# Performance work log

Measured on AMD Instinct MI355X. Metric: run time of the kernel, lower is better.

Reference implementation:

```python
import jax, jax.numpy as jnp
from jax import lax
import numpy as np

DN = ('NCHW', 'OIHW', 'NCHW')


def conv(x, w, b, pad=0):
    y = lax.conv_general_dilated(x, w, (1, 1), [(pad, pad), (pad, pad)],
                                 dimension_numbers=DN)
    return y + b[None, :, None, None]


def deconv(x, w, b, stride=1):
    # PyTorch ConvTranspose2d weight is (in, out, kH, kW); equivalent conv uses
    # flipped, in/out-transposed kernel with lhs dilation = stride, pad = k-1.
    k = w.shape[2]
    wt = jnp.flip(w, (2, 3)).transpose(1, 0, 2, 3)
    y = lax.conv_general_dilated(x, wt, (1, 1), [(k - 1, k - 1), (k - 1, k - 1)],
                                 lhs_dilation=(stride, stride), dimension_numbers=DN)
    return y + b[None, :, None, None]


def maxpool2(x):
    return lax.reduce_window(x, -jnp.inf, lax.max, (1, 1, 2, 2), (1, 1, 2, 2), 'VALID')


def setup_inputs() -> dict:
    key = jax.random.key(0)
    ks = jax.random.split(key, 12)
    B = 256

    def he(k, shape, fan_in):
        return jax.random.normal(k, shape, jnp.float32) * np.sqrt(2.0 / fan_in)

    inp = {
        'x': jax.random.normal(ks[0], (B, 1, 28, 28), jnp.float32),
        # encoder convs
        'w1': he(ks[1], (128, 1, 5, 5), 1 * 25), 'b1': jnp.zeros((128,), jnp.float32),
        'w2': he(ks[2], (128, 128, 5, 5), 128 * 25), 'b2': jnp.zeros((128,), jnp.float32),
        'w3': he(ks[3], (128, 128, 5, 5), 128 * 25), 'b3': jnp.zeros((128,), jnp.float32),
        # decoder transposed convs (torch shape: in, out, kH, kW)
        't1w': he(ks[4], (128, 128, 4, 4), 128 * 16), 't1b': jnp.zeros((128,), jnp.float32),
        't2w': he(ks[5], (128, 128, 4, 4), 128 * 16), 't2b': jnp.zeros((128,), jnp.float32),
        't3w': he(ks[6], (128, 128, 5, 5), 128 * 25), 't3b': jnp.zeros((128,), jnp.float32),
        't4w': he(ks[7], (128, 128, 5, 5), 128 * 25), 't4b': jnp.zeros((128,), jnp.float32),
        # mu_net 1x1 conv
        'mw': he(ks[8], (1, 128, 1, 1), 128), 'mb': jnp.zeros((1,), jnp.float32),
        # codebook: Embedding(128, 128), init ~ N(0, 1)
        'dict_w': jax.random.normal(ks[9], (128, 128), jnp.float32),
    }
    return inp


def reference(x, w1, b1, w2, b2, w3, b3,
              t1w, t1b, t2w, t2b, t3w, t3b, t4w, t4b,
              mw, mb, dict_w):
    BETA, RATE = 0.25, 5.0
    # ---- encoder ----
    h = jax.nn.relu(conv(x, w1, b1, pad=0))          # (B,128,24,24)
    h = jax.nn.relu(conv(h, w2, b2, pad=2))          # (B,128,24,24)
    h = maxpool2(h)                                  # (B,128,12,12)
    h = conv(h, w3, b3, pad=2)                       # (B,128,12,12)
    z = maxpool2(h)                                  # (B,128,6,6)

    # ---- nearest_neighbor (faithful: argmax of distance, as in the source) ----
    z_sg = lax.stop_gradient(z)
    z2 = jnp.sum(z_sg * z_sg, axis=1, keepdims=True)          # (B,1,6,6)
    w2n = jnp.sum(dict_w * dict_w, axis=1)                     # (K,)
    cross = jnp.einsum('bchw,kc->bkhw', z_sg, lax.stop_gradient(dict_w))
    d2 = z2 + w2n[None, :, None, None] - 2.0 * cross           # (B,K,6,6)
    index = jnp.argmax(d2, axis=1)                             # (B,6,6) int

    # ---- embedding gather ----
    val = dict_w[index].transpose(0, 3, 1, 2)                  # (B,128,6,6)

    # ---- decoder on detached codes ----
    f = lax.stop_gradient(val)
    f = jax.nn.relu(deconv(f, t1w, t1b, stride=1))             # (B,128,9,9)
    f = jax.nn.relu(deconv(f, t2w, t2b, stride=2))             # (B,128,20,20)
    f = jax.nn.relu(deconv(f, t3w, t3b, stride=1))             # (B,128,24,24)
    f = jax.nn.relu(deconv(f, t4w, t4b, stride=1))             # (B,128,28,28)
    mu = conv(f, mw, mb, pad=0)                                # (B,1,28,28)

    loss_rec = jnp.mean((mu - x) ** 2)
    dict_loss = jnp.mean((val - lax.stop_gradient(z)) ** 2) * RATE
    enc_loss = jnp.mean((z - lax.stop_gradient(val)) ** 2) * BETA * RATE
    var_loss = jnp.zeros((), jnp.float32)
    losses = jnp.stack([loss_rec, dict_loss, enc_loss, var_loss])
    return losses, index
```

## Files before the change

kernel.cpp:

```cpp
#include <hip/hip_runtime.h>
#include <hip/hip_bf16.h>


#define B_ 256

typedef __attribute__((ext_vector_type(8))) short s16x8;
typedef __attribute__((ext_vector_type(4))) short s16x4;
typedef __attribute__((ext_vector_type(8))) _Float16 f16x8;
typedef __attribute__((ext_vector_type(4))) float f32x4;

__device__ inline ushort f2bf(float f) {
  union { __hip_bfloat16 h; ushort u; } cv;
  cv.h = __float2bfloat16(f);
  return cv.u;
}

__global__ __launch_bounds__(256) void prep_w(const float* __restrict__ w,
                                              ushort* __restrict__ wp,
                                              int K2) {
  int idx = blockIdx.x * 256 + threadIdx.x;
  if (idx >= K2 * 16384) return;
  int ci = idx & 127;
  int co = (idx >> 7) & 127;
  int tap = idx >> 14;
  wp[idx] = f2bf(w[((size_t)ci * 128 + co) * K2 + (K2 - 1 - tap)]);
}

__global__ __launch_bounds__(256) void prep_w_s2(const float* __restrict__ w,
                                                 ushort* __restrict__ wp) {
  int idx = blockIdx.x * 256 + threadIdx.x;
  int ci = idx & 127;
  int co = (idx >> 7) & 127;
  int tap = (idx >> 14) & 3;
  int pp = idx >> 16;
  int u = tap >> 1, v = tap & 1;
  int py = pp >> 1, px = pp & 1;
  wp[idx] =
      f2bf(w[(((size_t)ci * 128 + co) * 4 + (py + 2 * u)) * 4 + (px + 2 * v)]);
}

__global__ __launch_bounds__(256) void prep_w_split(const float* __restrict__ w,
                                                    _Float16* __restrict__ wh,
                                                    _Float16* __restrict__ wl,
                                                    int K2) {
  int idx = blockIdx.x * 256 + threadIdx.x;
  if (idx >= K2 * 16384) return;
  int ci = idx & 127;
  int co = (idx >> 7) & 127;
  int tap = idx >> 14;
  float v = w[((size_t)co * 128 + ci) * K2 + tap];
  _Float16 h = (_Float16)v;
  wh[idx] = h;
  wl[idx] = (_Float16)(v - (float)h);
}

__global__ __launch_bounds__(256) void conv1_kernel(
    const float* __restrict__ x, const float* __restrict__ w,
    const float* __restrict__ b, _Float16* __restrict__ oh,
    _Float16* __restrict__ ol) {
  const int n = blockIdx.x;
  __shared__ float xl[784];
  __shared__ float wl[128 * 25];
  __shared__ float bl[128];
  const int t = threadIdx.x;
  for (int e = t; e < 784; e += 256) xl[e] = x[n * 784 + e];
  for (int e = t; e < 3200; e += 256) wl[e] = w[e];
  if (t < 128) bl[t] = b[t];
  __syncthreads();
  const size_t nb = (size_t)n * 73728;
  for (int idx = t; idx < 73728; idx += 256) {
    int co = idx & 127, p = idx >> 7;
    int y = p / 24, xx = p % 24;
    float acc = bl[co];
    const float* wc = &wl[co * 25];
#pragma unroll
    for (int ky = 0; ky < 5; ky++)
#pragma unroll
      for (int kx = 0; kx < 5; kx++)
        acc += xl[(y + ky) * 28 + xx + kx] * wc[ky * 5 + kx];
    float v = fmaxf(acc, 0.f);
    _Float16 h = (_Float16)v;
    oh[nb + idx] = h;
    ol[nb + idx] = (_Float16)(v - (float)h);
  }
}

template <int IW, int K, int PAD, int TR, bool RELU, bool OUT_F32>
__global__ __launch_bounds__(256, 3) void conv_mfma_pool(
    const _Float16* __restrict__ inh, const _Float16* __restrict__ inl,
    const _Float16* __restrict__ wph, const _Float16* __restrict__ wpl,
    const float* __restrict__ bias, _Float16* __restrict__ outh,
    _Float16* __restrict__ outl, float* __restrict__ outf) {
  constexpr int IH = IW, OW = IW, OH = IW;
  constexpr int PW = IW + 2 * PAD;
  constexpr int SROWS = TR + K - 1;
  constexpr int S = SROWS * PW;
  constexpr int NPOS = TR * OW;
  constexpr int NCH = NPOS / 16;
  constexpr int K2 = K * K;
  constexpr int PITCH = 40;
  constexpr int LIN_ELT = S * PITCH;
  constexpr int LIN_BYTES = 2 * LIN_ELT * 2;
  constexpr int SCR_BYTES = 64 * NPOS * 4;
  constexpr int SMEM_BYTES = LIN_BYTES > SCR_BYTES ? LIN_BYTES : SCR_BYTES;
  static_assert(NPOS % 16 == 0, "");
  static_assert(TR % 2 == 0 && OW % 2 == 0, "");
  __shared__ __align__(16) char smem[SMEM_BYTES];
  _Float16* linh = (_Float16*)smem;
  _Float16* linl = linh + LIN_ELT;
  const int n = blockIdx.x;
  const int r0 = blockIdx.y * TR;
  const int t = threadIdx.x;
  const int wv = t >> 6;
  const int lane = t & 63;
  const int nn = lane & 15;
  const int q = lane >> 4;
  f32x4 acc0[NCH], acc1[NCH];
#pragma unroll
  for (int c = 0; c < NCH; c++) {
    acc0[c] = f32x4{0.f, 0.f, 0.f, 0.f};
    acc1[c] = f32x4{0.f, 0.f, 0.f, 0.f};
  }
  int base[NCH];
#pragma unroll
  for (int c = 0; c < NCH; c++) {
    int p = c * 16 + nn;
    base[c] = (p / OW) * PW + (p % OW);
  }
  const int rowA = wv * 16 + nn;
  const int rowB = (wv + 4) * 16 + nn;
  for (int cb = 0; cb < 4; cb++) {
    const int ci0 = cb * 32;
    __syncthreads();
    for (int e = t; e < S * 4; e += 256) {
      int sp = e >> 2, j = e & 3;
      int r = sp / PW, c = sp - r * PW;
      int ir = r0 + r - PAD, ic = c - PAD;
      f16x8 vh = {0, 0, 0, 0, 0, 0, 0, 0};
      f16x8 vl = {0, 0, 0, 0, 0, 0, 0, 0};
      if (ir >= 0 && ir < IH && ic >= 0 && ic < IW) {
        size_t g = ((size_t)n * (IH * IW) + ir * IW + ic) * 128 + ci0 + j * 8;
        vh = *(const f16x8*)&inh[g];
        vl = *(const f16x8*)&inl[g];
      }
      int st = sp * PITCH + ((j + (sp >> 3)) & 3) * 8;
      *(f16x8*)&linh[st] = vh;
      *(f16x8*)&linl[st] = vl;
    }
    __syncthreads();
    const size_t gA = (size_t)rowA * 128 + ci0 + q * 8;
    const size_t gB = (size_t)rowB * 128 + ci0 + q * 8;
    f16x8 cah0 = *(const f16x8*)&wph[gA];
    f16x8 cal0 = *(const f16x8*)&wpl[gA];
    f16x8 cah1 = *(const f16x8*)&wph[gB];
    f16x8 cal1 = *(const f16x8*)&wpl[gB];
    for (int tap = 0; tap < K2; tap++) {
      f16x8 nah0 = cah0, nal0 = cal0, nah1 = cah1, nal1 = cal1;
      if (tap + 1 < K2) {
        size_t oA = gA + (size_t)(tap + 1) * 16384;
        size_t oB = gB + (size_t)(tap + 1) * 16384;
        nah0 = *(const f16x8*)&wph[oA];
        nal0 = *(const f16x8*)&wpl[oA];
        nah1 = *(const f16x8*)&wph[oB];
        nal1 = *(const f16x8*)&wpl[oB];
      }
      const int ky = tap / K, kx = tap - ky * K;
      const int toff = ky * PW + kx;
#pragma unroll
      for (int c = 0; c < NCH; c++) {
        int s = base[c] + toff;
        int off = s * PITCH + ((q + (s >> 3)) & 3) * 8;
        f16x8 bh = *(const f16x8*)&linh[off];
        f16x8 bl = *(const f16x8*)&linl[off];
        acc0[c] =
            __builtin_amdgcn_mfma_f32_16x16x32_f16(cah0, bh, acc0[c], 0, 0, 0);
        acc0[c] =
            __builtin_amdgcn_mfma_f32_16x16x32_f16(cah0, bl, acc0[c], 0, 0, 0);
        acc0[c] =
            __builtin_amdgcn_mfma_f32_16x16x32_f16(cal0, bh, acc0[c], 0, 0, 0);
        acc1[c] =
            __builtin_amdgcn_mfma_f32_16x16x32_f16(cah1, bh, acc1[c], 0, 0, 0);
        acc1[c] =
            __builtin_amdgcn_mfma_f32_16x16x32_f16(cah1, bl, acc1[c], 0, 0, 0);
        acc1[c] =
            __builtin_amdgcn_mfma_f32_16x16x32_f16(cal1, bh, acc1[c], 0, 0, 0);
      }
      cah0 = nah0; cal0 = nal0; cah1 = nah1; cal1 = nal1;
    }
  }
  __syncthreads();
  float* scr = (float*)smem + wv * 16 * NPOS;
#pragma unroll
  for (int j = 0; j < 2; j++) {
    const int cot = (j ? wv + 4 : wv) * 16;
#pragma unroll
    for (int c = 0; c < NCH; c++) {
      f32x4 a = j ? acc1[c] : acc0[c];
#pragma unroll
      for (int r = 0; r < 4; r++) {
        float v = a[r] + bias[cot + q * 4 + r];
        if (RELU) v = fmaxf(v, 0.f);
        scr[(q * 4 + r) * NPOS + c * 16 + nn] = v;
      }
    }
    __syncthreads();
    for (int e = lane; e < 16 * (TR / 2) * (OW / 2); e += 64) {
      int co_l = e & 15;
      int rem = e >> 4;
      int pr = rem / (OW / 2), pc = rem - pr * (OW / 2);
      const float* s = scr + co_l * NPOS;
      int lp = (2 * pr) * OW + 2 * pc;
      float m =
          fmaxf(fmaxf(s[lp], s[lp + 1]), fmaxf(s[lp + OW], s[lp + OW + 1]));
      int sp_out = (r0 / 2 + pr) * (OW / 2) + pc;
      size_t go = ((size_t)n * ((OH / 2) * (OW / 2)) + sp_out) * 128 + cot + co_l;
      if (OUT_F32) {
        outf[go] = m;
      } else {
        _Float16 h = (_Float16)m;
        outh[go] = h;
        outl[go] = (_Float16)(m - (float)h);
      }
    }
    __syncthreads();
  }
}

__global__ __launch_bounds__(256) void vq_kernel(
    const float* __restrict__ z, const float* __restrict__ dict,
    float* __restrict__ val, ushort* __restrict__ val_bf,
    float* __restrict__ out_idx) {
  const int n = blockIdx.x;
  __shared__ float zl[36 * 128];
  __shared__ float d2[36 * 129];
  __shared__ float w2n[128];
  __shared__ int bk[36];
  const int t = threadIdx.x;
  const float* zn = z + (size_t)n * 4608;
  for (int e = t; e < 4608; e += 256) zl[e] = zn[e];
  if (t < 128) {
    float s = 0.f;
    const float* wr = dict + t * 128;
    for (int c = 0; c < 128; c++) s += wr[c] * wr[c];
    w2n[t] = s;
  }
  __syncthreads();
  const int k = t & 127, pg = t >> 7;
  float dot[18];
#pragma unroll
  for (int i = 0; i < 18; i++) dot[i] = 0.f;
  const float* wr = dict + k * 128;
  for (int c = 0; c < 128; c++) {
    float wv = wr[c];
#pragma unroll
    for (int i = 0; i < 18; i++) dot[i] += zl[(pg * 18 + i) * 128 + c] * wv;
  }
  float wn = w2n[k];
#pragma unroll
  for (int i = 0; i < 18; i++) d2[(pg * 18 + i) * 129 + k] = wn - 2.f * dot[i];
  __syncthreads();
  if (t < 36) {
    const float* dr = &d2[t * 129];
    float best = dr[0];
    int bi = 0;
    for (int kk = 1; kk < 128; kk++) {
      float v = dr[kk];
      if (v > best) { best = v; bi = kk; }
    }
    bk[t] = bi;
    out_idx[n * 36 + t] = (float)bi;
  }
  __syncthreads();
  float* vn = val + (size_t)n * 4608;
  ushort* vbn = val_bf + (size_t)n * 4608;
  for (int e = t; e < 4608; e += 256) {
    int c = e & 127, p = e >> 7;
    float v = dict[bk[p] * 128 + c];
    vn[e] = v;
    vbn[e] = f2bf(v);
  }
}

template <int IH, int IW, int OH, int OW, int K, int TR, bool MU_FUSE>
__global__ __launch_bounds__(256, 3) void deconv_mfma(
    const ushort* __restrict__ in, const ushort* __restrict__ wprep,
    const float* __restrict__ bias, const float* __restrict__ mw,
    void* __restrict__ outp) {
  constexpr int PAD = K - 1;
  constexpr int PW = IW + 2 * PAD;
  constexpr int K2 = K * K;
  constexpr int SROWS = TR + K - 1;
  constexpr int S = SROWS * PW;
  constexpr int NPOS = TR * OW;
  constexpr int NCH = (NPOS + 15) / 16;
  constexpr int PITCH = 40;
  const int n = blockIdx.x;
  const int r0 = blockIdx.y * TR;
  __shared__ __align__(16) ushort lin[S * PITCH];
  const int t = threadIdx.x;
  const int wv = t >> 6;
  const int lane = t & 63;
  const int nn = lane & 15;
  const int q = lane >> 4;
  f32x4 acc0[NCH], acc1[NCH];
  int base[NCH];
#pragma unroll
  for (int c = 0; c < NCH; c++) {
    acc0[c] = f32x4{0.f, 0.f, 0.f, 0.f};
    acc1[c] = f32x4{0.f, 0.f, 0.f, 0.f};
    int p = c * 16 + nn;
    int pc = p < NPOS ? p : NPOS - 1;
    base[c] = (pc / OW) * PW + (pc % OW);
  }
  for (int cb = 0; cb < 4; cb++) {
    const int ci0 = cb * 32;
    __syncthreads();
    for (int e = t; e < S * 4; e += 256) {
      int sp = e >> 2, j = e & 3;
      int rr = sp / PW, cc = sp - rr * PW;
      int ir = r0 + rr - PAD, ic = cc - PAD;
      s16x8 v = {0, 0, 0, 0, 0, 0, 0, 0};
      if (ir >= 0 && ir < IH && ic >= 0 && ic < IW)
        v = *(const s16x8*)&in[((size_t)n * (IH * IW) + ir * IW + ic) * 128 +
                               ci0 + j * 8];
      *(s16x8*)&lin[sp * PITCH + ((j + (sp >> 3)) & 3) * 8] = v;
    }
    __syncthreads();
    const size_t gA = (size_t)(wv * 16 + nn) * 128 + ci0 + q * 8;
    const size_t gB = (size_t)((wv + 4) * 16 + nn) * 128 + ci0 + q * 8;
    s16x8 ca0 = *(const s16x8*)&wprep[gA];
    s16x8 ca1 = *(const s16x8*)&wprep[gB];
    for (int tap = 0; tap < K2; tap++) {
      s16x8 na0 = ca0, na1 = ca1;
      if (tap + 1 < K2) {
        na0 = *(const s16x8*)&wprep[gA + (size_t)(tap + 1) * 16384];
        na1 = *(const s16x8*)&wprep[gB + (size_t)(tap + 1) * 16384];
      }
      const int ky = tap / K, kx = tap - ky * K;
      const int toff = ky * PW + kx;
#pragma unroll
      for (int c = 0; c < NCH; c++) {
        int s = base[c] + toff;
        s16x8 b = *(const s16x8*)&lin[s * PITCH + ((q + (s >> 3)) & 3) * 8];
        acc0[c] =
            __builtin_amdgcn_mfma_f32_16x16x32_bf16(ca0, b, acc0[c], 0, 0, 0);
        acc1[c] =
            __builtin_amdgcn_mfma_f32_16x16x32_bf16(ca1, b, acc1[c], 0, 0, 0);
      }
      ca0 = na0; ca1 = na1;
    }
  }
  const int co_a = wv * 16 + q * 4;
  const int co_b = (wv + 4) * 16 + q * 4;
  float ba[4], bb[4];
#pragma unroll
  for (int r = 0; r < 4; r++) {
    ba[r] = bias[co_a + r];
    bb[r] = bias[co_b + r];
  }
  if (!MU_FUSE) {
    ushort* out = (ushort*)outp;
#pragma unroll
    for (int c = 0; c < NCH; c++) {
      int p = c * 16 + nn;
      if (p < NPOS) {
        size_t go = ((size_t)n * (OH * OW) + r0 * OW + p) * 128;
        s16x4 pa, pb;
#pragma unroll
        for (int r = 0; r < 4; r++) {
          pa[r] = (short)f2bf(fmaxf(acc0[c][r] + ba[r], 0.f));
          pb[r] = (short)f2bf(fmaxf(acc1[c][r] + bb[r], 0.f));
        }
        *(s16x4*)&out[go + co_a] = pa;
        *(s16x4*)&out[go + co_b] = pb;
      }
    }
  } else {
    float* out = (float*)outp;
    float wa[4], wb[4];
#pragma unroll
    for (int r = 0; r < 4; r++) {
      wa[r] = mw[co_a + r];
      wb[r] = mw[co_b + r];
    }
#pragma unroll
    for (int c = 0; c < NCH; c++) {
      int p = c * 16 + nn;
      float s = 0.f;
#pragma unroll
      for (int r = 0; r < 4; r++) {
        s += fmaxf(acc0[c][r] + ba[r], 0.f) * wa[r];
        s += fmaxf(acc1[c][r] + bb[r], 0.f) * wb[r];
      }
      s += __shfl_xor(s, 16);
      s += __shfl_xor(s, 32);
      if (q == 0 && p < NPOS)
        atomicAdd(&out[(size_t)n * (OH * OW) + r0 * OW + p], s);
    }
  }
}

__global__ __launch_bounds__(256, 3) void deconv_s2_mfma(
    const ushort* __restrict__ in, const ushort* __restrict__ wp2,
    const float* __restrict__ bias, ushort* __restrict__ out) {
  constexpr int NCH = 7;
  constexpr int PITCH = 40;
  const int n = blockIdx.x;
  const int pp = blockIdx.y;
  const int py = pp >> 1, px = pp & 1;
  __shared__ __align__(16) ushort lin[121 * PITCH];
  const int t = threadIdx.x;
  const int wv = t >> 6;
  const int lane = t & 63;
  const int nn = lane & 15;
  const int q = lane >> 4;
  f32x4 acc0[NCH], acc1[NCH];
  int base[NCH];
#pragma unroll
  for (int c = 0; c < NCH; c++) {
    acc0[c] = f32x4{0.f, 0.f, 0.f, 0.f};
    acc1[c] = f32x4{0.f, 0.f, 0.f, 0.f};
    int p = c * 16 + nn;
    int pc = p < 100 ? p : 99;
    base[c] = (pc / 10) * 11 + (pc % 10);
  }
  const int toffs[4] = {12, 11, 1, 0};
  for (int cb = 0; cb < 4; cb++) {
    const int ci0 = cb * 32;
    __syncthreads();
    for (int e = t; e < 121 * 4; e += 256) {
      int sp = e >> 2, j = e & 3;
      int r = sp / 11, c2 = sp - r * 11;
      int ir = r - 1, ic = c2 - 1;
      s16x8 v = {0, 0, 0, 0, 0, 0, 0, 0};
      if (ir >= 0 && ir < 9 && ic >= 0 && ic < 9)
        v = *(const s16x8*)&in[((size_t)n * 81 + ir * 9 + ic) * 128 + ci0 +
                               j * 8];
      *(s16x8*)&lin[sp * PITCH + ((j + (sp >> 3)) & 3) * 8] = v;
    }
    __syncthreads();
    const size_t gA =
        ((size_t)(pp * 4) * 128 + wv * 16 + nn) * 128 + ci0 + q * 8;
    const size_t gB =
        ((size_t)(pp * 4) * 128 + (wv + 4) * 16 + nn) * 128 + ci0 + q * 8;
    s16x8 ca0 = *(const s16x8*)&wp2[gA];
    s16x8 ca1 = *(const s16x8*)&wp2[gB];
    for (int tap = 0; tap < 4; tap++) {
      s16x8 na0 = ca0, na1 = ca1;
      if (tap + 1 < 4) {
        na0 = *(const s16x8*)&wp2[gA + (size_t)(tap + 1) * 16384];
        na1 = *(const s16x8*)&wp2[gB + (size_t)(tap + 1) * 16384];
      }
      const int toff = toffs[tap];
#pragma unroll
      for (int c = 0; c < NCH; c++) {
        int s = base[c] + toff;
        s16x8 b = *(const s16x8*)&lin[s * PITCH + ((q + (s >> 3)) & 3) * 8];
        acc0[c] =
            __builtin_amdgcn_mfma_f32_16x16x32_bf16(ca0, b, acc0[c], 0, 0, 0);
        acc1[c] =
            __builtin_amdgcn_mfma_f32_16x16x32_bf16(ca1, b, acc1[c], 0, 0, 0);
      }
      ca0 = na0; ca1 = na1;
    }
  }
  const int co_a = wv * 16 + q * 4;
  const int co_b = (wv + 4) * 16 + q * 4;
#pragma unroll
  for (int c = 0; c < NCH; c++) {
    int p = c * 16 + nn;
    if (p < 100) {
      int oy = 2 * (p / 10) + py, ox = 2 * (p % 10) + px;
      size_t go = ((size_t)n * 400 + oy * 20 + ox) * 128;
      s16x4 pa, pb;
#pragma unroll
      for (int r = 0; r < 4; r++) {
        pa[r] = (short)f2bf(fmaxf(acc0[c][r] + bias[co_a + r], 0.f));
        pb[r] = (short)f2bf(fmaxf(acc1[c][r] + bias[co_b + r], 0.f));
      }
      *(s16x4*)&out[go + co_a] = pa;
      *(s16x4*)&out[go + co_b] = pb;
    }
  }
}

__global__ __launch_bounds__(256) void rec_loss_kernel(
    const float* __restrict__ mu, const float* __restrict__ mb,
    const float* __restrict__ x, float* __restrict__ out) {
  const int t = threadIdx.x;
  const int i = blockIdx.x * 256 + t;
  __shared__ float red[256];
  float d = mu[i] + mb[0] - x[i];
  red[t] = d * d;
  __syncthreads();
  for (int off = 128; off > 0; off >>= 1) {
    if (t < off) red[t] += red[t + off];
    __syncthreads();
  }
  if (t == 0) atomicAdd(out, red[0] * (1.0f / 200704.f));
}

__global__ __launch_bounds__(256) void vq_loss_kernel(
    const float4* __restrict__ val4, const float4* __restrict__ z4,
    float* __restrict__ out) {
  const int t = threadIdx.x;
  const int i = blockIdx.x * 256 + t;
  __shared__ float red[256];
  float4 a = val4[i], b = z4[i];
  float dx = a.x - b.x, dy = a.y - b.y, dz = a.z - b.z, dw = a.w - b.w;
  red[t] = dx * dx + dy * dy + dz * dz + dw * dw;
  __syncthreads();
  for (int off = 128; off > 0; off >>= 1) {
    if (t < off) red[t] += red[t + off];
    __syncthreads();
  }
  if (t == 0) {
    atomicAdd(out + 1, red[0] * (5.f / 1179648.f));
    atomicAdd(out + 2, red[0] * (1.25f / 1179648.f));
  }
}

extern "C" void kernel_launch(void* const* d_in, const int* in_sizes, int n_in,
                              void* d_out, int out_size, void* d_ws,
                              size_t ws_size, hipStream_t stream) {
  const float* x = (const float*)d_in[0];
  const float* w1 = (const float*)d_in[1];
  const float* b1 = (const float*)d_in[2];
  const float* w2 = (const float*)d_in[3];
  const float* b2 = (const float*)d_in[4];
  const float* w3 = (const float*)d_in[5];
  const float* b3 = (const float*)d_in[6];
  const float* t1w = (const float*)d_in[7];
  const float* t1b = (const float*)d_in[8];
  const float* t2w = (const float*)d_in[9];
  const float* t2b = (const float*)d_in[10];
  const float* t3w = (const float*)d_in[11];
  const float* t3b = (const float*)d_in[12];
  const float* t4w = (const float*)d_in[13];
  const float* t4b = (const float*)d_in[14];
  const float* mw = (const float*)d_in[15];
  const float* mb = (const float*)d_in[16];
  const float* dictw = (const float*)d_in[17];
  float* out = (float*)d_out;

  float* p = (float*)d_ws;
  _Float16* h1h = (_Float16*)p; p += 9437184;
  _Float16* h1l = (_Float16*)p; p += 9437184;
  _Float16* p1h = (_Float16*)p; p += 2359296;
  _Float16* p1l = (_Float16*)p; p += 2359296;
  float* z = p; p += 1179648;
  float* val = p; p += 1179648;
  ushort* val_bf = (ushort*)p; p += 589824;
  float* mu = p; p += 200704;
  ushort* wp1 = (ushort*)p; p += 131072;
  ushort* wp3 = (ushort*)p; p += 204800;
  ushort* wp4 = (ushort*)p; p += 204800;
  ushort* wp2 = (ushort*)p; p += 131072;
  _Float16* w2h = (_Float16*)p; p += 204800;
  _Float16* w2l = (_Float16*)p; p += 204800;
  _Float16* w3h = (_Float16*)p; p += 204800;
  _Float16* w3l = (_Float16*)p; p += 204800;
  ushort* f1 = (ushort*)p1h;
  ushort* f2 = (ushort*)h1l;
  ushort* f3 = (ushort*)h1h;

  hipMemsetAsync(d_out, 0, 4 * sizeof(float), stream);
  hipMemsetAsync(mu, 0, 200704 * sizeof(float), stream);

  prep_w<<<16 * 64, 256, 0, stream>>>(t1w, wp1, 16);
  prep_w<<<25 * 64, 256, 0, stream>>>(t3w, wp3, 25);
  prep_w<<<25 * 64, 256, 0, stream>>>(t4w, wp4, 25);
  prep_w_s2<<<1024, 256, 0, stream>>>(t2w, wp2);
  prep_w_split<<<25 * 64, 256, 0, stream>>>(w2, w2h, w2l, 25);
  prep_w_split<<<25 * 64, 256, 0, stream>>>(w3, w3h, w3l, 25);

  conv1_kernel<<<B_, 256, 0, stream>>>(x, w1, b1, h1h, h1l);
  conv_mfma_pool<24, 5, 2, 6, true, false>
      <<<dim3(B_, 4), 256, 0, stream>>>(h1h, h1l, w2h, w2l, b2, p1h, p1l,
                                        nullptr);
  conv_mfma_pool<12, 5, 2, 4, false, true>
      <<<dim3(B_, 3), 256, 0, stream>>>(p1h, p1l, w3h, w3l, b3, nullptr,
                                        nullptr, z);
  vq_kernel<<<B_, 256, 0, stream>>>(z, dictw, val, val_bf, out + 4);
  deconv_mfma<6, 6, 9, 9, 4, 9, false>
      <<<dim3(B_, 1), 256, 0, stream>>>(val_bf, wp1, t1b, nullptr, f1);
  deconv_s2_mfma<<<dim3(B_, 4), 256, 0, stream>>>(f1, wp2, t2b, f2);
  deconv_mfma<20, 20, 24, 24, 5, 8, false>
      <<<dim3(B_, 3), 256, 0, stream>>>(f2, wp3, t3b, nullptr, f3);
  deconv_mfma<24, 24, 28, 28, 5, 7, true>
      <<<dim3(B_, 4), 256, 0, stream>>>(f3, wp4, t4b, mw, mu);
  rec_loss_kernel<<<784, 256, 0, stream>>>(mu, mb, x, out);
  vq_loss_kernel<<<1152, 256, 0, stream>>>((const float4*)val, (const float4*)z,
                                           out);
}
```

Baseline: 1.011 ms.

## Double-buffer LDS input staging in conv/deconv, merge prep and loss kernels

The conv and deconv MFMA kernels now prefetch the next 32-channel input slice into registers while computing on the current slice, then store it into a second LDS buffer. This removes one barrier per channel block and overlaps global loads with MFMA work. Launch bounds drop from 3 to 2 blocks per SM to make room for the doubled shared memory and staging registers. Conv2 switches from 6-row to 4-row tiles, and the six weight-prep kernels and the two loss kernels are each merged into one launch. Together these cut launch overhead at some cost in occupancy.

```diff
diff --git a/kernel.cpp b/kernel.cpp
--- a/kernel.cpp
+++ b/kernel.cpp
@@ -15,43 +15,49 @@
   return cv.u;
 }
 
-__global__ __launch_bounds__(256) void prep_w(const float* __restrict__ w,
-                                              ushort* __restrict__ wp,
-                                              int K2) {
-  int idx = blockIdx.x * 256 + threadIdx.x;
-  if (idx >= K2 * 16384) return;
-  int ci = idx & 127;
-  int co = (idx >> 7) & 127;
-  int tap = idx >> 14;
-  wp[idx] = f2bf(w[((size_t)ci * 128 + co) * K2 + (K2 - 1 - tap)]);
-}
-
-__global__ __launch_bounds__(256) void prep_w_s2(const float* __restrict__ w,
-                                                 ushort* __restrict__ wp) {
-  int idx = blockIdx.x * 256 + threadIdx.x;
-  int ci = idx & 127;
-  int co = (idx >> 7) & 127;
-  int tap = (idx >> 14) & 3;
-  int pp = idx >> 16;
-  int u = tap >> 1, v = tap & 1;
-  int py = pp >> 1, px = pp & 1;
-  wp[idx] =
-      f2bf(w[(((size_t)ci * 128 + co) * 4 + (py + 2 * u)) * 4 + (px + 2 * v)]);
-}
-
-__global__ __launch_bounds__(256) void prep_w_split(const float* __restrict__ w,
-                                                    _Float16* __restrict__ wh,
-                                                    _Float16* __restrict__ wl,
-                                                    int K2) {
-  int idx = blockIdx.x * 256 + threadIdx.x;
-  if (idx >= K2 * 16384) return;
-  int ci = idx & 127;
-  int co = (idx >> 7) & 127;
-  int tap = idx >> 14;
-  float v = w[((size_t)co * 128 + ci) * K2 + tap];
-  _Float16 h = (_Float16)v;
-  wh[idx] = h;
-  wl[idx] = (_Float16)(v - (float)h);
+__global__ __launch_bounds__(256) void prep_all(
+    const float* __restrict__ t1w, const float* __restrict__ t3w,
+    const float* __restrict__ t4w, const float* __restrict__ t2w,
+    const float* __restrict__ w2, const float* __restrict__ w3,
+    ushort* __restrict__ wp1, ushort* __restrict__ wp3,
+    ushort* __restrict__ wp4, ushort* __restrict__ wp2,
+    _Float16* __restrict__ w2h, _Float16* __restrict__ w2l,
+    _Float16* __restrict__ w3h, _Float16* __restrict__ w3l) {
+  const int b = blockIdx.x, t = threadIdx.x;
+  if (b < 1024) {
+    int idx = b * 256 + t;
+    int ci = idx & 127, co = (idx >> 7) & 127, tap = idx >> 14;
+    wp1[idx] = f2bf(t1w[((size_t)ci * 128 + co) * 16 + (15 - tap)]);
+  } else if (b < 2624) {
+    int idx = (b - 1024) * 256 + t;
+    int ci = idx & 127, co = (idx >> 7) & 127, tap = idx >> 14;
+    wp3[idx] = f2bf(t3w[((size_t)ci * 128 + co) * 25 + (24 - tap)]);
+  } else if (b < 4224) {
+    int idx = (b - 2624) * 256 + t;
+    int ci = idx & 127, co = (idx >> 7) & 127, tap = idx >> 14;
+    wp4[idx] = f2bf(t4w[((size_t)ci * 128 + co) * 25 + (24 - tap)]);
+  } else if (b < 5248) {
+    int idx = (b - 4224) * 256 + t;
+    int ci = idx & 127, co = (idx >> 7) & 127;
+    int tap = (idx >> 14) & 3, pp = idx >> 16;
+    int u = tap >> 1, v = tap & 1, py = pp >> 1, px = pp & 1;
+    wp2[idx] = f2bf(
+        t2w[(((size_t)ci * 128 + co) * 4 + (py + 2 * u)) * 4 + (px + 2 * v)]);
+  } else if (b < 6848) {
+    int idx = (b - 5248) * 256 + t;
+    int ci = idx & 127, co = (idx >> 7) & 127, tap = idx >> 14;
+    float v = w2[((size_t)co * 128 + ci) * 25 + tap];
+    _Float16 h = (_Float16)v;
+    w2h[idx] = h;
+    w2l[idx] = (_Float16)(v - (float)h);
+  } else {
+    int idx = (b - 6848) * 256 + t;
+    int ci = idx & 127, co = (idx >> 7) & 127, tap = idx >> 14;
+    float v = w3[((size_t)co * 128 + ci) * 25 + tap];
+    _Float16 h = (_Float16)v;
+    w3h[idx] = h;
+    w3l[idx] = (_Float16)(v - (float)h);
+  }
 }
 
 __global__ __launch_bounds__(256) void conv1_kernel(
@@ -86,7 +92,7 @@
 }
 
 template <int IW, int K, int PAD, int TR, bool RELU, bool OUT_F32>
-__global__ __launch_bounds__(256, 3) void conv_mfma_pool(
+__global__ __launch_bounds__(256, 2) void conv_mfma_pool(
     const _Float16* __restrict__ inh, const _Float16* __restrict__ inl,
     const _Float16* __restrict__ wph, const _Float16* __restrict__ wpl,
     const float* __restrict__ bias, _Float16* __restrict__ outh,
@@ -100,14 +106,14 @@
   constexpr int K2 = K * K;
   constexpr int PITCH = 40;
   constexpr int LIN_ELT = S * PITCH;
-  constexpr int LIN_BYTES = 2 * LIN_ELT * 2;
+  constexpr int BUF_BYTES = 2 * LIN_ELT * 2;
+  constexpr int LIN_BYTES = 2 * BUF_BYTES;
   constexpr int SCR_BYTES = 64 * NPOS * 4;
   constexpr int SMEM_BYTES = LIN_BYTES > SCR_BYTES ? LIN_BYTES : SCR_BYTES;
+  constexpr int NSTG = (S * 4 + 255) / 256;
   static_assert(NPOS % 16 == 0, "");
   static_assert(TR % 2 == 0 && OW % 2 == 0, "");
   __shared__ __align__(16) char smem[SMEM_BYTES];
-  _Float16* linh = (_Float16*)smem;
-  _Float16* linl = linh + LIN_ELT;
   const int n = blockIdx.x;
   const int r0 = blockIdx.y * TR;
   const int t = threadIdx.x;
@@ -129,25 +135,51 @@
   }
   const int rowA = wv * 16 + nn;
   const int rowB = (wv + 4) * 16 + nn;
+  f16x8 sh[NSTG], sl[NSTG];
+
+  auto load_stage = [&](int ci0) {
+#pragma unroll
+    for (int i = 0; i < NSTG; i++) {
+      int e = t + i * 256;
+      f16x8 vh = {0, 0, 0, 0, 0, 0, 0, 0};
+      f16x8 vl = {0, 0, 0, 0, 0, 0, 0, 0};
+      if (e < S * 4) {
+        int sp = e >> 2, j = e & 3;
+        int r = sp / PW, c = sp - r * PW;
+        int ir = r0 + r - PAD, ic = c - PAD;
+        if (ir >= 0 && ir < IH && ic >= 0 && ic < IW) {
+          size_t g = ((size_t)n * (IH * IW) + ir * IW + ic) * 128 + ci0 + j * 8;
+          vh = *(const f16x8*)&inh[g];
+          vl = *(const f16x8*)&inl[g];
+        }
+      }
+      sh[i] = vh;
+      sl[i] = vl;
+    }
+  };
+  auto store_stage = [&](int bsel) {
+    _Float16* lh = (_Float16*)(smem + bsel * BUF_BYTES);
+    _Float16* ll = lh + LIN_ELT;
+#pragma unroll
+    for (int i = 0; i < NSTG; i++) {
+      int e = t + i * 256;
+      if (e < S * 4) {
+        int sp = e >> 2, j = e & 3;
+        int st = sp * PITCH + ((j + (sp >> 3)) & 3) * 8;
+        *(f16x8*)&lh[st] = sh[i];
+        *(f16x8*)&ll[st] = sl[i];
+      }
+    }
+  };
+
+  load_stage(0);
+  store_stage(0);
+  __syncthreads();
   for (int cb = 0; cb < 4; cb++) {
     const int ci0 = cb * 32;
-    __syncthreads();
-    for (int e = t; e < S * 4; e += 256) {
-      int sp = e >> 2, j = e & 3;
-      int r = sp / PW, c = sp - r * PW;
-      int ir = r0 + r - PAD, ic = c - PAD;
-      f16x8 vh = {0, 0, 0, 0, 0, 0, 0, 0};
-      f16x8 vl = {0, 0, 0, 0, 0, 0, 0, 0};
-      if (ir >= 0 && ir < IH && ic >= 0 && ic < IW) {
-        size_t g = ((size_t)n * (IH * IW) + ir * IW + ic) * 128 + ci0 + j * 8;
-        vh = *(const f16x8*)&inh[g];
-        vl = *(const f16x8*)&inl[g];
-      }
-      int st = sp * PITCH + ((j + (sp >> 3)) & 3) * 8;
-      *(f16x8*)&linh[st] = vh;
-      *(f16x8*)&linl[st] = vl;
-    }
-    __syncthreads();
+    if (cb < 3) load_stage(ci0 + 32);
+    const _Float16* lh = (const _Float16*)(smem + (cb & 1) * BUF_BYTES);
+    const _Float16* ll = lh + LIN_ELT;
     const size_t gA = (size_t)rowA * 128 + ci0 + q * 8;
     const size_t gB = (size_t)rowB * 128 + ci0 + q * 8;
     f16x8 cah0 = *(const f16x8*)&wph[gA];
@@ -170,8 +202,8 @@
       for (int c = 0; c < NCH; c++) {
         int s = base[c] + toff;
         int off = s * PITCH + ((q + (s >> 3)) & 3) * 8;
-        f16x8 bh = *(const f16x8*)&linh[off];
-        f16x8 bl = *(const f16x8*)&linl[off];
+        f16x8 bh = *(const f16x8*)&lh[off];
+        f16x8 bl = *(const f16x8*)&ll[off];
         acc0[c] =
             __builtin_amdgcn_mfma_f32_16x16x32_f16(cah0, bh, acc0[c], 0, 0, 0);
         acc0[c] =
@@ -187,6 +219,10 @@
       }
       cah0 = nah0; cal0 = nal0; cah1 = nah1; cal1 = nal1;
     }
+    if (cb < 3) {
+      store_stage((cb + 1) & 1);
+      __syncthreads();
+    }
   }
   __syncthreads();
   float* scr = (float*)smem + wv * 16 * NPOS;
@@ -213,7 +249,8 @@
       float m =
           fmaxf(fmaxf(s[lp], s[lp + 1]), fmaxf(s[lp + OW], s[lp + OW + 1]));
       int sp_out = (r0 / 2 + pr) * (OW / 2) + pc;
-      size_t go = ((size_t)n * ((OH / 2) * (OW / 2)) + sp_out) * 128 + cot + co_l;
+      size_t go =
+          ((size_t)n * ((OH / 2) * (OW / 2)) + sp_out) * 128 + cot + co_l;
       if (OUT_F32) {
         outf[go] = m;
       } else {
@@ -282,7 +319,7 @@
 }
 
 template <int IH, int IW, int OH, int OW, int K, int TR, bool MU_FUSE>
-__global__ __launch_bounds__(256, 3) void deconv_mfma(
+__global__ __launch_bounds__(256, 2) void deconv_mfma(
     const ushort* __restrict__ in, const ushort* __restrict__ wprep,
     const float* __restrict__ bias, const float* __restrict__ mw,
     void* __restrict__ outp) {
@@ -294,9 +331,11 @@
   constexpr int NPOS = TR * OW;
   constexpr int NCH = (NPOS + 15) / 16;
   constexpr int PITCH = 40;
+  constexpr int LIN_ELT = S * PITCH;
+  constexpr int NSTG = (S * 4 + 255) / 256;
+  __shared__ __align__(16) ushort lin[2][LIN_ELT];
   const int n = blockIdx.x;
   const int r0 = blockIdx.y * TR;
-  __shared__ __align__(16) ushort lin[S * PITCH];
   const int t = threadIdx.x;
   const int wv = t >> 6;
   const int lane = t & 63;
@@ -312,20 +351,41 @@
     int pc = p < NPOS ? p : NPOS - 1;
     base[c] = (pc / OW) * PW + (pc % OW);
   }
+  s16x8 stg[NSTG];
+  auto load_stage = [&](int ci0) {
+#pragma unroll
+    for (int i = 0; i < NSTG; i++) {
+      int e = t + i * 256;
+      s16x8 v = {0, 0, 0, 0, 0, 0, 0, 0};
+      if (e < S * 4) {
+        int sp = e >> 2, j = e & 3;
+        int rr = sp / PW, cc = sp - rr * PW;
+        int ir = r0 + rr - PAD, ic = cc - PAD;
+        if (ir >= 0 && ir < IH && ic >= 0 && ic < IW)
+          v = *(const s16x8*)&in[((size_t)n * (IH * IW) + ir * IW + ic) * 128 +
+                                 ci0 + j * 8];
+      }
+      stg[i] = v;
+    }
+  };
+  auto store_stage = [&](int bsel) {
+#pragma unroll
+    for (int i = 0; i < NSTG; i++) {
+      int e = t + i * 256;
+      if (e < S * 4) {
+        int sp = e >> 2, j = e & 3;
+        *(s16x8*)&lin[bsel][sp * PITCH + ((j + (sp >> 3)) & 3) * 8] = stg[i];
+      }
+    }
+  };
+
+  load_stage(0);
+  store_stage(0);
+  __syncthreads();
   for (int cb = 0; cb < 4; cb++) {
     const int ci0 = cb * 32;
-    __syncthreads();
-    for (int e = t; e < S * 4; e += 256) {
-      int sp = e >> 2, j = e & 3;
-      int rr = sp / PW, cc = sp - rr * PW;
-      int ir = r0 + rr - PAD, ic = cc - PAD;
-      s16x8 v = {0, 0, 0, 0, 0, 0, 0, 0};
-      if (ir >= 0 && ir < IH && ic >= 0 && ic < IW)
-        v = *(const s16x8*)&in[((size_t)n * (IH * IW) + ir * IW + ic) * 128 +
-                               ci0 + j * 8];
-      *(s16x8*)&lin[sp * PITCH + ((j + (sp >> 3)) & 3) * 8] = v;
-    }
-    __syncthreads();
+    if (cb < 3) load_stage(ci0 + 32);
+    const ushort* L = lin[cb & 1];
     const size_t gA = (size_t)(wv * 16 + nn) * 128 + ci0 + q * 8;
     const size_t gB = (size_t)((wv + 4) * 16 + nn) * 128 + ci0 + q * 8;
     s16x8 ca0 = *(const s16x8*)&wprep[gA];
@@ -341,13 +401,17 @@
 #pragma unroll
       for (int c = 0; c < NCH; c++) {
         int s = base[c] + toff;
-        s16x8 b = *(const s16x8*)&lin[s * PITCH + ((q + (s >> 3)) & 3) * 8];
+        s16x8 b = *(const s16x8*)&L[s * PITCH + ((q + (s >> 3)) & 3) * 8];
         acc0[c] =
             __builtin_amdgcn_mfma_f32_16x16x32_bf16(ca0, b, acc0[c], 0, 0, 0);
         acc1[c] =
             __builtin_amdgcn_mfma_f32_16x16x32_bf16(ca1, b, acc1[c], 0, 0, 0);
       }
       ca0 = na0; ca1 = na1;
+    }
+    if (cb < 3) {
+      store_stage((cb + 1) & 1);
+      __syncthreads();
     }
   }
   const int co_a = wv * 16 + q * 4;
@@ -484,39 +548,34 @@
   }
 }
 
-__global__ __launch_bounds__(256) void rec_loss_kernel(
+__global__ __launch_bounds__(256) void loss_kernel(
     const float* __restrict__ mu, const float* __restrict__ mb,
-    const float* __restrict__ x, float* __restrict__ out) {
-  const int t = threadIdx.x;
-  const int i = blockIdx.x * 256 + t;
+    const float* __restrict__ x, const float4* __restrict__ val4,
+    const float4* __restrict__ z4, float* __restrict__ out) {
+  const int b = blockIdx.x, t = threadIdx.x;
   __shared__ float red[256];
-  float d = mu[i] + mb[0] - x[i];
-  red[t] = d * d;
+  if (b < 784) {
+    int i = b * 256 + t;
+    float d = mu[i] + mb[0] - x[i];
+    red[t] = d * d;
+  } else {
+    int i = (b - 784) * 256 + t;
+    float4 a = val4[i], zz = z4[i];
+    float dx = a.x - zz.x, dy = a.y - zz.y, dz = a.z - zz.z, dw = a.w - zz.w;
+    red[t] = dx * dx + dy * dy + dz * dz + dw * dw;
+  }
   __syncthreads();
   for (int off = 128; off > 0; off >>= 1) {
     if (t < off) red[t] += red[t + off];
     __syncthreads();
   }
-  if (t == 0) atomicAdd(out, red[0] * (1.0f / 200704.f));
-}
-
-__global__ __launch_bounds__(256) void vq_loss_kernel(
-    const float4* __restrict__ val4, const float4* __restrict__ z4,
-    float* __restrict__ out) {
-  const int t = threadIdx.x;
-  const int i = blockIdx.x * 256 + t;
-  __shared__ float red[256];
-  float4 a = val4[i], b = z4[i];
-  float dx = a.x - b.x, dy = a.y - b.y, dz = a.z - b.z, dw = a.w - b.w;
-  red[t] = dx * dx + dy * dy + dz * dz + dw * dw;
-  __syncthreads();
-  for (int off = 128; off > 0; off >>= 1) {
-    if (t < off) red[t] += red[t + off];
-    __syncthreads();
-  }
   if (t == 0) {
-    atomicAdd(out + 1, red[0] * (5.f / 1179648.f));
-    atomicAdd(out + 2, red[0] * (1.25f / 1179648.f));
+    if (b < 784) {
+      atomicAdd(out, red[0] * (1.0f / 200704.f));
+    } else {
+      atomicAdd(out + 1, red[0] * (5.f / 1179648.f));
+      atomicAdd(out + 2, red[0] * (1.25f / 1179648.f));
+    }
   }
 }
 
@@ -567,16 +626,12 @@
   hipMemsetAsync(d_out, 0, 4 * sizeof(float), stream);
   hipMemsetAsync(mu, 0, 200704 * sizeof(float), stream);
 
-  prep_w<<<16 * 64, 256, 0, stream>>>(t1w, wp1, 16);
-  prep_w<<<25 * 64, 256, 0, stream>>>(t3w, wp3, 25);
-  prep_w<<<25 * 64, 256, 0, stream>>>(t4w, wp4, 25);
-  prep_w_s2<<<1024, 256, 0, stream>>>(t2w, wp2);
-  prep_w_split<<<25 * 64, 256, 0, stream>>>(w2, w2h, w2l, 25);
-  prep_w_split<<<25 * 64, 256, 0, stream>>>(w3, w3h, w3l, 25);
+  prep_all<<<8448, 256, 0, stream>>>(t1w, t3w, t4w, t2w, w2, w3, wp1, wp3, wp4,
+                                     wp2, w2h, w2l, w3h, w3l);
 
   conv1_kernel<<<B_, 256, 0, stream>>>(x, w1, b1, h1h, h1l);
-  conv_mfma_pool<24, 5, 2, 6, true, false>
-      <<<dim3(B_, 4), 256, 0, stream>>>(h1h, h1l, w2h, w2l, b2, p1h, p1l,
+  conv_mfma_pool<24, 5, 2, 4, true, false>
+      <<<dim3(B_, 6), 256, 0, stream>>>(h1h, h1l, w2h, w2l, b2, p1h, p1l,
                                         nullptr);
   conv_mfma_pool<12, 5, 2, 4, false, true>
       <<<dim3(B_, 3), 256, 0, stream>>>(p1h, p1l, w3h, w3l, b3, nullptr,
@@ -589,7 +644,6 @@
       <<<dim3(B_, 3), 256, 0, stream>>>(f2, wp3, t3b, nullptr, f3);
   deconv_mfma<24, 24, 28, 28, 5, 7, true>
       <<<dim3(B_, 4), 256, 0, stream>>>(f3, wp4, t4b, mw, mu);
-  rec_loss_kernel<<<784, 256, 0, stream>>>(mu, mb, x, out);
-  vq_loss_kernel<<<1152, 256, 0, stream>>>((const float4*)val, (const float4*)z,
-                                           out);
-}
+  loss_kernel<<<1936, 256, 0, stream>>>(mu, mb, x, (const float4*)val,
+                                        (const float4*)z, out);
+}
```

Result: faster. 988.9 us (-2.2%).
